# Kernel optimization log

Measured on AMD Instinct MI355X. Metric: run time of the kernel, lower is better.

The kernel has to match this reference:

```python
import jax, jax.numpy as jnp
import numpy as np

B, IMG, TXT, N, FF, HID, C, E = 1024, 512, 300, 14, 2048, 128, 14, 182
D = IMG + TXT  # 812, transformer d_model


def setup_inputs() -> dict:
    key = jax.random.key(0)
    ks = jax.random.split(key, 12)
    r = lambda k, s, sc=0.02: (jax.random.normal(k, s, jnp.float32) * sc)
    return {
        "img_feat": jax.random.normal(ks[0], (B, IMG), jnp.float32),
        "word_embeds": jax.random.normal(ks[1], (N, TXT), jnp.float32),
        "edge_index": jax.random.randint(ks[2], (2, E), 0, N, jnp.int32),
        "in_proj_w": r(ks[3], (3 * D, D)),
        "in_proj_b": jnp.zeros((3 * D,), jnp.float32),
        "out_proj_w": r(ks[4], (D, D)),
        "out_proj_b": jnp.zeros((D,), jnp.float32),
        "ln1_g": jnp.ones((D,), jnp.float32), "ln1_b": jnp.zeros((D,), jnp.float32),
        "ln2_g": jnp.ones((D,), jnp.float32), "ln2_b": jnp.zeros((D,), jnp.float32),
        "ffn_w1": r(ks[5], (D, FF)), "ffn_b1": jnp.zeros((FF,), jnp.float32),
        "ffn_w2": r(ks[6], (FF, D)), "ffn_b2": jnp.zeros((D,), jnp.float32),
        "gcn1_w": r(ks[7], (D, HID)), "gcn1_b": jnp.zeros((HID,), jnp.float32),
        "gcn2_w": r(ks[8], (HID, HID)), "gcn2_b": jnp.zeros((HID,), jnp.float32),
        "lin_w": r(ks[9], (HID, C)), "lin_b": jnp.zeros((C,), jnp.float32),
    }


def layer_norm(x, g, b, eps=1e-5):
    mu = x.mean(-1, keepdims=True)
    var = ((x - mu) ** 2).mean(-1, keepdims=True)
    return (x - mu) * jax.lax.rsqrt(var + eps) * g + b


def gcn_conv(x, edge_index, W, b, n_nodes):
    # PyG GCNConv: add self loops, symmetric normalization, x @ W then scatter-add.
    # x: (B, N, F_in); gather/scatter along node axis (node_dim=-2).
    src, dst = edge_index[0], edge_index[1]
    loop = jnp.arange(n_nodes, dtype=src.dtype)
    src = jnp.concatenate([src, loop])
    dst = jnp.concatenate([dst, loop])
    deg = jnp.zeros((n_nodes,), x.dtype).at[dst].add(1.0)
    dinv = jnp.where(deg > 0, deg ** -0.5, 0.0)
    ew = dinv[src] * dinv[dst]                       # (E+N,)
    h = x @ W                                        # (B, N, F_out)
    msg = h[:, src, :] * ew[None, :, None]           # gather neighbors
    out = jnp.zeros_like(h).at[:, dst, :].add(msg)   # scatter-aggregate
    return out + b


def reference(img_feat, word_embeds, edge_index,
              in_proj_w, in_proj_b, out_proj_w, out_proj_b,
              ln1_g, ln1_b, ln2_g, ln2_b,
              ffn_w1, ffn_b1, ffn_w2, ffn_b2,
              gcn1_w, gcn1_b, gcn2_w, gcn2_b, lin_w, lin_b):
    # Broadcast image feature across the 14 label nodes; concat word embeddings.
    node = jnp.concatenate([
        jnp.broadcast_to(img_feat[:, None, :], (B, N, IMG)),
        jnp.broadcast_to(word_embeds[None, :, :], (B, N, TXT)),
    ], axis=-1)                                      # (B, N, D)

    # torch TransformerEncoderLayer, batch_first=False, nhead=1, post-norm, relu.
    # Input (B, N, D) is interpreted as (seq=B, batch=N, D): attention over dim 0.
    qkv = node @ in_proj_w.T + in_proj_b
    q, k, v = jnp.split(qkv, 3, axis=-1)             # each (B, N, D)
    scale = 1.0 / jnp.sqrt(jnp.asarray(D, node.dtype))
    scores = jnp.einsum('lnd,mnd->nlm', q, k) * scale  # (N, B, B)
    attn = jax.nn.softmax(scores, axis=-1)
    ao = jnp.einsum('nlm,mnd->lnd', attn, v)           # (B, N, D)
    ao = ao @ out_proj_w.T + out_proj_b
    x = layer_norm(node + ao, ln1_g, ln1_b)
    ff = jax.nn.relu(x @ ffn_w1 + ffn_b1) @ ffn_w2 + ffn_b2
    x = layer_norm(x + ff, ln2_g, ln2_b)               # (B, N, D)

    # Two GCNConv layers over the 14-node label graph (batched over B).
    x = jax.nn.relu(gcn_conv(x, edge_index, gcn1_w, gcn1_b, N))
    x = gcn_conv(x, edge_index, gcn2_w, gcn2_b, N)
    x = jax.nn.relu(x.mean(axis=1))                    # mean over nodes -> (B, HID)
    return x @ lin_w + lin_b                           # (B, C)
```

## Files before the change

### kernel.cpp

```cpp
#include <hip/hip_runtime.h>
#include <math.h>

#define B_    1024
#define IMG_  512
#define TXT_  300
#define NN_   14
#define FF_   2048
#define HID_  128
#define CC_   14
#define EE_   182
#define DD_   812
#define D3_   2436
#define BNR_  14336
#define KP_   832
#define TXP_  320
#define AROWS_ 1152

typedef __bf16 bf16x8 __attribute__((ext_vector_type(8)));
typedef float  f32x4  __attribute__((ext_vector_type(4)));
typedef unsigned short u16;

__device__ __forceinline__ u16 f2bf(float f) {
    union { float f; unsigned u; } v; v.f = f;
    unsigned r = v.u + 0x7FFFu + ((v.u >> 16) & 1u);
    return (u16)(r >> 16);
}
__device__ __forceinline__ float bf2f(u16 h) {
    union { unsigned u; float f; } v; v.u = ((unsigned)h) << 16; return v.f;
}

__device__ __forceinline__ void gload_lds16(const u16* g, u16* l) {
    __builtin_amdgcn_global_load_lds(
        (const __attribute__((address_space(1))) void*)g,
        (__attribute__((address_space(3))) void*)l, 16, 0, 0);
}

#define OFF_IMGB  0ULL
#define OFF_WIB   1048576ULL
#define OFF_WORDB 3543040ULL
#define OFF_WITX  3624960ULL
#define OFF_GB    0ULL
#define OFF_EBUF  29360128ULL
#define OFF_AVOT  33611776ULL
#define OFF_WOB   35446784ULL
#define OFF_HB    0ULL
#define OFF_PB    58720256ULL
#define OFF_X1B   82001920ULL
#define OFF_YB    105857024ULL
#define OFF_W1T   129712128ULL
#define OFF_W2T   133120000ULL
#define OFF_AQB   152420352ULL
#define OFF_TVB   158307552ULL
#define OFF_CO    158520544ULL
#define OFF_Z     158566016ULL
#define OFF_ADJ   158623360ULL
#define OFF_WG1T  158624384ULL
#define OFF_WG2T  158837376ULL

__device__ __forceinline__ void gemm_body(
    const u16* __restrict__ A, int lda,
    const u16* __restrict__ Bm, int ldb,
    int M, int N, int K, float scale,
    float* __restrict__ Cf, int ldc,
    u16* __restrict__ Cb, int ldcb,
    const float* __restrict__ bias,
    int nxt, int swiz, int epi, int id)
{
    __shared__ __align__(16) u16 As[2][128 * 32];
    __shared__ __align__(16) u16 Bs[2][128 * 32];
    const int tid = threadIdx.x;
    int bx, by;
    if (swiz) { int r8 = id & 7; int q = id >> 3; bx = q % nxt; by = (q / nxt) * 8 + r8; }
    else      { bx = id % nxt; by = id / nxt; }
    const int row0 = by * 128, col0 = bx * 128;
    const int lane = tid & 63, wv = tid >> 6;
    const int wm = (wv >> 1) * 32, wn = (wv & 1) * 64;
    const int fr = lane & 15, qd = lane >> 4;

    const int s_row = tid >> 2;
    const int s_ko  = (tid & 3) * 8;
    const int s_b0  = wv * 512;
    const u16* Arow = A  + (size_t)(row0 + s_row) * lda + s_ko;
    const u16* Brow = Bm + (size_t)(col0 + s_row) * ldb + s_ko;

    f32x4 acc[2][4] = {};

    const int T = K >> 5;
    gload_lds16(Arow, &As[0][s_b0]);
    gload_lds16(Brow, &Bs[0][s_b0]);

    for (int i = 0; i < T; ++i) {
        __syncthreads();
        const int cur = i & 1;
        if (i + 1 < T) {
            const int ko = (i + 1) << 5;
            gload_lds16(Arow + ko, &As[cur ^ 1][s_b0]);
            gload_lds16(Brow + ko, &Bs[cur ^ 1][s_b0]);
        }
        bf16x8 af[2], bg[4];
        #pragma unroll
        for (int j = 0; j < 2; ++j)
            af[j] = *(const bf16x8*)&As[cur][(wm + j * 16 + fr) * 32 + qd * 8];
        #pragma unroll
        for (int j = 0; j < 4; ++j)
            bg[j] = *(const bf16x8*)&Bs[cur][(wn + j * 16 + fr) * 32 + qd * 8];
        #pragma unroll
        for (int mi = 0; mi < 2; ++mi)
            #pragma unroll
            for (int ni = 0; ni < 4; ++ni)
                acc[mi][ni] = __builtin_amdgcn_mfma_f32_16x16x32_bf16(
                    af[mi], bg[ni], acc[mi][ni], 0, 0, 0);
    }

    #pragma unroll
    for (int mi = 0; mi < 2; ++mi) {
        #pragma unroll
        for (int i = 0; i < 4; ++i) {
            int rm = row0 + wm + mi * 16 + qd * 4 + i;
            if (rm >= M) continue;
            #pragma unroll
            for (int ni = 0; ni < 4; ++ni) {
                int cn = col0 + wn + ni * 16 + fr;
                if (cn >= N) continue;
                float v = acc[mi][ni][i] * scale;
                if (epi == 0) Cf[(size_t)rm * ldc + cn] = v;
                else if (epi == 1) { v += bias[cn]; v = v > 0.f ? v : 0.f;
                                Cb[(size_t)rm * ldcb + cn] = f2bf(v); }
                else if (epi == 2) Cf[(size_t)rm * ldc + cn] =
                                v + bias[cn] + bf2f(Cb[(size_t)rm * ldcb + cn]);
                else if (epi == 3) Cb[(size_t)rm * ldcb + cn] = f2bf(v);
                else if (epi == 4) { int bs = cn / DD_, cc = cn - bs * DD_;
                                Cb[(size_t)bs * (AROWS_ * KP_) + (size_t)rm * KP_ + cc] = f2bf(v); }
                else if (epi == 5) { float invz = 1.0f / bias[rm];
                                Cb[(size_t)rm * ldcb + cn] = f2bf(v * invz); }
                else if (epi == 6) Cf[(size_t)rm * ldc + cn] = v + bias[cn];
                else if (epi == 7) { const u16* rx = (const u16*)Cf;
                                Cb[(size_t)rm * ldcb + cn] =
                                    f2bf(v + bias[cn] + bf2f(rx[(size_t)rm * ldc + cn])); }
                else if (epi == 8) {
                    float t = v + bias[cn];
                    if (cn < DD_) Cb[(size_t)(1024 + rm) * KP_ + cn] = f2bf(t);
                    else if (cn >= 2 * DD_)
                        ((u16*)Cf)[(size_t)rm * KP_ + (cn - 2 * DD_)] = f2bf(t);
                }
            }
        }
    }
}

template<int EPI>
__global__ __launch_bounds__(512, 6)
void bgemm(const u16* __restrict__ A, int lda,
           const u16* __restrict__ Bm, int ldb,
           int M, int N, int K, float scale,
           float* __restrict__ Cf, int ldc,
           u16* __restrict__ Cb, int ldcb,
           const float* __restrict__ bias,
           int nxt, int swiz)
{
    gemm_body(A, lda, Bm, ldb, M, N, K, scale, Cf, ldc, Cb, ldcb, bias,
              nxt, swiz, EPI, blockIdx.x);
}

struct GDesc {
    const u16* A; const u16* B; float* Cf; u16* Cb; const float* bias;
    int lda, ldb, ldc, ldcb, M, N, K, epi, nxt, swiz, blk0;
    float scale;
};
struct TDesc { const float* src; u16* dst; int srs, drs, rows, cols, padrows, rt, nblk; };
struct MPack { GDesc g[3]; TDesc t[2]; const int* ei; float* Adj; int ng, gtot, nt; };

__device__ __forceinline__ void castT_body(TDesc T, int id)
{
    __shared__ float t[32][33];
    const int bx = id % T.rt, by = id / T.rt;
    const int r0 = bx * 32, c0 = by * 32;
    const int tx = threadIdx.x & 31, ty = threadIdx.x >> 5;
    #pragma unroll
    for (int k = 0; k < 2; ++k) {
        int r = r0 + ty + k * 16, c = c0 + tx;
        t[ty + k * 16][tx] = (r < T.rows && c < T.cols) ? T.src[(size_t)r * T.srs + c] : 0.f;
    }
    __syncthreads();
    #pragma unroll
    for (int k = 0; k < 2; ++k) {
        int c = c0 + ty + k * 16, r = r0 + tx;
        if (c < T.cols && r < T.padrows)
            T.dst[(size_t)c * T.drs + r] = f2bf(t[tx][ty + k * 16]);
    }
}

__device__ __forceinline__ void adj_body(const int* __restrict__ ei, float* __restrict__ Adj)
{
    if (threadIdx.x != 0) return;
    float deg[NN_];
    for (int i = 0; i < NN_; ++i) deg[i] = 1.f;
    for (int e = 0; e < EE_; ++e) deg[ei[EE_ + e]] += 1.f;
    float dinv[NN_];
    for (int i = 0; i < NN_; ++i) dinv[i] = rsqrtf(deg[i]);
    float adj[NN_ * NN_];
    for (int t = 0; t < NN_ * NN_; ++t) adj[t] = 0.f;
    for (int e = 0; e < EE_; ++e) {
        int s = ei[e], d = ei[EE_ + e];
        adj[d * NN_ + s] += dinv[s] * dinv[d];
    }
    for (int i = 0; i < NN_; ++i) adj[i * NN_ + i] += dinv[i] * dinv[i];
    for (int t = 0; t < NN_ * NN_; ++t) Adj[t] = adj[t];
    for (int i = 0; i < 16; ++i) {
        float s = 0.f;
        if (i < NN_) for (int j = 0; j < NN_; ++j) s += adj[j * NN_ + i];
        Adj[NN_ * NN_ + i] = s / (float)NN_;
    }
}

__global__ __launch_bounds__(512, 6)
void kern_mix(MPack p)
{
    int id = blockIdx.x;
    if (id < p.gtot) {
        int si = 0;
        for (int s = 1; s < p.ng; ++s) if (id >= p.g[s].blk0) si = s;
        GDesc D = p.g[si];
        gemm_body(D.A, D.lda, D.B, D.ldb, D.M, D.N, D.K, D.scale,
                  D.Cf, D.ldc, D.Cb, D.ldcb, D.bias, D.nxt, D.swiz, D.epi,
                  id - D.blk0);
        return;
    }
    id -= p.gtot;
    for (int s = 0; s < p.nt; ++s) {
        if (id < p.t[s].nblk) { castT_body(p.t[s], id); return; }
        id -= p.t[s].nblk;
    }
    if (id == 0 && p.ei) adj_body(p.ei, p.Adj);
}

struct CDesc { const float* src; u16* dst; int srs, drs, dcols, scols; };
struct CPack { CDesc d[9]; unsigned cum[10]; int n; };

__global__ void kern_mcast(CPack p)
{
    unsigned idx = blockIdx.x * 256 + threadIdx.x;
    int si = -1;
    for (int s = 0; s < p.n; ++s)
        if (idx >= p.cum[s] && idx < p.cum[s + 1]) { si = s; break; }
    if (si < 0) return;
    CDesc D = p.d[si];
    unsigned k = idx - p.cum[si];
    int r = k / D.dcols, c = k - r * D.dcols;
    D.dst[(size_t)r * D.drs + c] =
        (c < D.scols) ? f2bf(D.src[(size_t)r * D.srs + c]) : (u16)0;
}

__global__ __launch_bounds__(256) void kern_eG(const float* __restrict__ S,
    u16* __restrict__ Gb, float* __restrict__ Z)
{
    __shared__ float red[256];
    __shared__ u16 ews[NN_ * 1024];
    const int l = blockIdx.x, tid = threadIdx.x;
    const int lane = tid & 63, wv = tid >> 6;

    const float* wraw = S + 1024 * 1024;
    for (int z = wv; z < NN_; z += 4) {
        const float* r = wraw + z * 1024;
        float vv[16], mx = -1e30f;
        #pragma unroll
        for (int j = 0; j < 16; ++j) { vv[j] = r[lane + 64 * j]; mx = fmaxf(mx, vv[j]); }
        #pragma unroll
        for (int off = 32; off > 0; off >>= 1) mx = fmaxf(mx, __shfl_down(mx, off));
        mx = __shfl(mx, 0);
        #pragma unroll
        for (int j = 0; j < 16; ++j)
            ews[z * 1024 + lane + 64 * j] = f2bf(expf(vv[j] - mx));
    }
    const float* row = S + (size_t)l * 1024;
    float m = -1e30f;
    #pragma unroll
    for (int k = 0; k < 4; ++k) m = fmaxf(m, row[tid + 256 * k]);
    red[tid] = m; __syncthreads();
    for (int s = 128; s > 0; s >>= 1) {
        if (tid < s) red[tid] = fmaxf(red[tid], red[tid + s]);
        __syncthreads();
    }
    m = red[0];
    float ev[16];
    #pragma unroll
    for (int j = 0; j < 16; ++j) ev[j] = expf(row[lane + 64 * j] - m);
    u16* gr = Gb + (size_t)l * NN_ * 1024;
    for (int z = wv; z < NN_; z += 4) {
        const u16* er = &ews[z * 1024];
        float s = 0.f;
        #pragma unroll
        for (int j = 0; j < 16; ++j) {
            float pv = ev[j] * bf2f(er[lane + 64 * j]);
            gr[(size_t)z * 1024 + lane + 64 * j] = f2bf(pv);
            s += pv;
        }
        #pragma unroll
        for (int off = 32; off > 0; off >>= 1) s += __shfl_down(s, off);
        if (lane == 0) Z[l * NN_ + z] = s;
    }
}

__global__ __launch_bounds__(256) void kern_ln1(
    const float* __restrict__ img, const float* __restrict__ word,
    const u16* __restrict__ Pb,
    const float* __restrict__ co, const float* __restrict__ g,
    const float* __restrict__ bta, u16* __restrict__ Xb)
{
    __shared__ float buf[DD_];
    __shared__ float red[256];
    __shared__ float stats[2];
    int row = blockIdx.x;
    int b = row / NN_, n = row - b * NN_;
    const u16* pr = Pb + (size_t)row * DD_;
    const float* cr = co + n * DD_;
    float s = 0.f;
    for (int d = threadIdx.x; d < DD_; d += 256) {
        float v = (d < IMG_) ? img[(size_t)b * IMG_ + d] : word[n * TXT_ + d - IMG_];
        v += bf2f(pr[d]) + cr[d];
        buf[d] = v; s += v;
    }
    red[threadIdx.x] = s; __syncthreads();
    for (int t = 128; t > 0; t >>= 1) {
        if (threadIdx.x < t) red[threadIdx.x] += red[threadIdx.x + t];
        __syncthreads();
    }
    if (threadIdx.x == 0) stats[0] = red[0] / DD_;
    __syncthreads();
    float mu = stats[0], s2 = 0.f;
    for (int d = threadIdx.x; d < DD_; d += 256) { float t = buf[d] - mu; s2 += t * t; }
    red[threadIdx.x] = s2; __syncthreads();
    for (int t = 128; t > 0; t >>= 1) {
        if (threadIdx.x < t) red[threadIdx.x] += red[threadIdx.x + t];
        __syncthreads();
    }
    if (threadIdx.x == 0) stats[1] = rsqrtf(red[0] / DD_ + 1e-5f);
    __syncthreads();
    float rstd = stats[1];
    u16* xb = Xb + (size_t)row * KP_;
    for (int d = threadIdx.x; d < DD_; d += 256)
        xb[d] = f2bf((buf[d] - mu) * rstd * g[d] + bta[d]);
    for (int d = DD_ + threadIdx.x; d < KP_; d += 256) xb[d] = 0;
}

#define X2S_ 840
#define G1S_ 136
__global__ __launch_bounds__(256, 4)
void kern_gcn(const u16* __restrict__ Yb,
              const float* __restrict__ g2v, const float* __restrict__ bt2,
              const u16* __restrict__ Wg1T, const float* __restrict__ bg1,
              const u16* __restrict__ Wg2T, const float* __restrict__ bg2,
              const float* __restrict__ Wl,  const float* __restrict__ bl,
              const float* __restrict__ AdjW, float* __restrict__ out)
{
    __shared__ __align__(16) u16 x2s[16 * X2S_];
    __shared__ __align__(16) float h1s[16 * 132];
    __shared__ float adj_s[NN_ * NN_];
    __shared__ float colw_s[16];
    __shared__ float pool_s[HID_];
    u16* g1s = x2s;
    const int b = blockIdx.x, tid = threadIdx.x;
    const int lane = tid & 63, wv = tid >> 6;
    const int fr = lane & 15, qd = lane >> 4;

    if (tid < NN_ * NN_) adj_s[tid] = AdjW[tid];
    if (tid >= NN_ * NN_ && tid < NN_ * NN_ + 16) colw_s[tid - NN_ * NN_] = AdjW[tid];
    for (int k = tid; k < 2 * X2S_; k += 256) x2s[14 * X2S_ + k] = 0;
    for (int k = tid; k < 14 * (X2S_ - DD_); k += 256) {
        int j = k / (X2S_ - DD_), c = k - j * (X2S_ - DD_);
        x2s[j * X2S_ + DD_ + c] = 0;
    }

    for (int j = wv; j < NN_; j += 4) {
        const u16* yr = Yb + (size_t)(b * NN_ + j) * KP_;
        float vv[13], s = 0.f;
        #pragma unroll
        for (int k = 0; k < 13; ++k) {
            int d = lane + 64 * k;
            float v = (d < DD_) ? bf2f(yr[d]) : 0.f;
            vv[k] = v; s += v;
        }
        #pragma unroll
        for (int off = 32; off > 0; off >>= 1) s += __shfl_down(s, off);
        s = __shfl(s, 0);
        float mu = s / (float)DD_, s2 = 0.f;
        #pragma unroll
        for (int k = 0; k < 13; ++k) {
            int d = lane + 64 * k;
            float t = (d < DD_) ? vv[k] - mu : 0.f;
            s2 += t * t;
        }
        #pragma unroll
        for (int off = 32; off > 0; off >>= 1) s2 += __shfl_down(s2, off);
        s2 = __shfl(s2, 0);
        float rstd = rsqrtf(s2 / (float)DD_ + 1e-5f);
        #pragma unroll
        for (int k = 0; k < 13; ++k) {
            int d = lane + 64 * k;
            if (d < DD_)
                x2s[j * X2S_ + d] = f2bf((vv[k] - mu) * rstd * g2v[d] + bt2[d]);
        }
    }
    __syncthreads();

    {
        f32x4 acc[2] = {{}, {}};
        const u16* wp0 = Wg1T + (size_t)(wv * 32 + fr) * KP_ + qd * 8;
        const u16* wp1 = wp0 + (size_t)16 * KP_;
        bf16x8 bc0 = *(const bf16x8*)wp0;
        bf16x8 bc1 = *(const bf16x8*)wp1;
        for (int k0 = 0; k0 < KP_; k0 += 32) {
            bf16x8 bn0 = bc0, bn1 = bc1;
            if (k0 + 32 < KP_) {
                bn0 = *(const bf16x8*)(wp0 + k0 + 32);
                bn1 = *(const bf16x8*)(wp1 + k0 + 32);
            }
            bf16x8 af = *(const bf16x8*)&x2s[fr * X2S_ + k0 + qd * 8];
            acc[0] = __builtin_amdgcn_mfma_f32_16x16x32_bf16(af, bc0, acc[0], 0, 0, 0);
            acc[1] = __builtin_amdgcn_mfma_f32_16x16x32_bf16(af, bc1, acc[1], 0, 0, 0);
            bc0 = bn0; bc1 = bn1;
        }
        #pragma unroll
        for (int t = 0; t < 2; ++t)
            #pragma unroll
            for (int i = 0; i < 4; ++i)
                h1s[(qd * 4 + i) * 132 + wv * 32 + t * 16 + fr] = acc[t][i];
    }
    __syncthreads();

    {
        const int f = tid & 127, jj = (tid >> 7) * 7;
        #pragma unroll
        for (int j = 0; j < 7; ++j) {
            float s = bg1[f];
            #pragma unroll
            for (int i = 0; i < NN_; ++i)
                s = fmaf(adj_s[(jj + j) * NN_ + i], h1s[i * 132 + f], s);
            g1s[(jj + j) * G1S_ + f] = f2bf(s > 0.f ? s : 0.f);
        }
        for (int k = tid; k < 2 * G1S_; k += 256) g1s[14 * G1S_ + k] = 0;
    }
    __syncthreads();

    {
        f32x4 acc[2] = {{}, {}};
        const u16* wp0 = Wg2T + (size_t)(wv * 32 + fr) * HID_ + qd * 8;
        const u16* wp1 = wp0 + (size_t)16 * HID_;
        bf16x8 bc0 = *(const bf16x8*)wp0;
        bf16x8 bc1 = *(const bf16x8*)wp1;
        for (int k0 = 0; k0 < HID_; k0 += 32) {
            bf16x8 bn0 = bc0, bn1 = bc1;
            if (k0 + 32 < HID_) {
                bn0 = *(const bf16x8*)(wp0 + k0 + 32);
                bn1 = *(const bf16x8*)(wp1 + k0 + 32);
            }
            bf16x8 af = *(const bf16x8*)&g1s[fr * G1S_ + k0 + qd * 8];
            acc[0] = __builtin_amdgcn_mfma_f32_16x16x32_bf16(af, bc0, acc[0], 0, 0, 0);
            acc[1] = __builtin_amdgcn_mfma_f32_16x16x32_bf16(af, bc1, acc[1], 0, 0, 0);
            bc0 = bn0; bc1 = bn1;
        }
        #pragma unroll
        for (int t = 0; t < 2; ++t) {
            float s = 0.f;
            #pragma unroll
            for (int i = 0; i < 4; ++i) s += colw_s[qd * 4 + i] * acc[t][i];
            s += __shfl_xor(s, 16);
            s += __shfl_xor(s, 32);
            if (qd == 0) {
                int f = wv * 32 + t * 16 + fr;
                float p = s + bg2[f];
                pool_s[f] = p > 0.f ? p : 0.f;
            }
        }
    }
    __syncthreads();

    if (tid < CC_) {
        float s = bl[tid];
        #pragma unroll 8
        for (int f = 0; f < HID_; ++f)
            s = fmaf(pool_s[f], Wl[(size_t)f * CC_ + tid], s);
        out[(size_t)b * CC_ + tid] = s;
    }
}

extern "C" void kernel_launch(void* const* d_in, const int* in_sizes, int n_in,
                              void* d_out, int out_size, void* d_ws, size_t ws_size,
                              hipStream_t stream)
{
    const float* img  = (const float*)d_in[0];
    const float* word = (const float*)d_in[1];
    const int*   ei   = (const int*)d_in[2];
    const float* Wi   = (const float*)d_in[3];
    const float* bi   = (const float*)d_in[4];
    const float* Wo   = (const float*)d_in[5];
    const float* bo   = (const float*)d_in[6];
    const float* g1   = (const float*)d_in[7];
    const float* bt1  = (const float*)d_in[8];
    const float* g2   = (const float*)d_in[9];
    const float* bt2  = (const float*)d_in[10];
    const float* W1   = (const float*)d_in[11];
    const float* bf1  = (const float*)d_in[12];
    const float* W2   = (const float*)d_in[13];
    const float* bf2  = (const float*)d_in[14];
    const float* Wg1  = (const float*)d_in[15];
    const float* bg1  = (const float*)d_in[16];
    const float* Wg2  = (const float*)d_in[17];
    const float* bg2  = (const float*)d_in[18];
    const float* Wl   = (const float*)d_in[19];
    const float* bl   = (const float*)d_in[20];
    float* out = (float*)d_out;

    char* ws = (char*)d_ws;
    u16*   imgb = (u16*)  (ws + OFF_IMGB);
    u16*   Wib  = (u16*)  (ws + OFF_WIB);
    u16*   wordb= (u16*)  (ws + OFF_WORDB);
    u16*   WiTX = (u16*)  (ws + OFF_WITX);
    u16*   Gb   = (u16*)  (ws + OFF_GB);
    float* Ebuf = (float*)(ws + OFF_EBUF);
    u16*   AvoT = (u16*)  (ws + OFF_AVOT);
    u16*   Wob  = (u16*)  (ws + OFF_WOB);
    u16*   Hb   = (u16*)  (ws + OFF_HB);
    u16*   Pb   = (u16*)  (ws + OFF_PB);
    u16*   X1b  = (u16*)  (ws + OFF_X1B);
    u16*   Yb   = (u16*)  (ws + OFF_YB);
    u16*   W1T  = (u16*)  (ws + OFF_W1T);
    u16*   W2T  = (u16*)  (ws + OFF_W2T);
    u16*   Aqb  = (u16*)  (ws + OFF_AQB);
    u16*   Akb  = Aqb + AROWS_ * KP_;
    u16*   Avb  = Aqb + 2 * AROWS_ * KP_;
    u16*   Tvb  = (u16*)  (ws + OFF_TVB);
    float* co   = (float*)(ws + OFF_CO);
    float* Zb   = (float*)(ws + OFF_Z);
    float* Adj  = (float*)(ws + OFF_ADJ);
    u16*   Wg1T = (u16*)  (ws + OFF_WG1T);
    u16*   Wg2T = (u16*)  (ws + OFF_WG2T);

    const float scl = 1.0f / sqrtf((float)DD_);

    {
        CPack p; p.n = 9;
        unsigned c = 0;
        auto seg = [&](int i, const float* s, int srs, u16* d, int drs,
                       int rows, int dcols, int scols) {
            p.d[i] = { s, d, srs, drs, dcols, scols };
            p.cum[i] = c; c += (unsigned)rows * dcols;
        };
        seg(0, img,        IMG_, imgb,  IMG_, B_,   IMG_, IMG_);
        seg(1, Wi,         DD_,  Wib,   IMG_, D3_,  IMG_, IMG_);
        seg(2, word,       TXT_, wordb, TXP_, NN_,  TXP_, TXT_);
        seg(3, Wi + IMG_,  DD_,  WiTX,  TXP_, D3_,  TXP_, TXT_);
        seg(4, Wo,         DD_,  Wob,   KP_,  DD_,  KP_,  DD_);
        seg(5, nullptr, 0, Aqb + DD_,                    KP_, 1038, 20, 0);
        seg(6, nullptr, 0, Aqb + AROWS_ * KP_ + DD_,     KP_, 1024, 20, 0);
        seg(7, nullptr, 0, Aqb + 2 * AROWS_ * KP_ + DD_, KP_, 1024, 20, 0);
        seg(8, nullptr, 0, Tvb + DD_,                    KP_, NN_,  20, 0);
        p.cum[9] = c;
        kern_mcast<<<(c + 255) / 256, 256, 0, stream>>>(p);
    }

    {
        MPack p{};
        p.ng = 2; p.gtot = 180;
        p.g[0] = { wordb, WiTX, (float*)Tvb, Aqb, bi,
                   TXP_, TXP_, 0, 0, NN_, D3_, TXP_, 8, 20, 0, 0, 1.f };
        p.g[1] = { imgb, Wib, nullptr, Aqb, nullptr,
                   IMG_, IMG_, 0, 0, B_, D3_, IMG_, 4, 20, 1, 20, 1.f };
        p.nt = 2;
        p.t[0] = { Wg1, Wg1T, HID_, KP_,  DD_,  HID_, KP_,  26, 26 * 4 };
        p.t[1] = { Wg2, Wg2T, HID_, HID_, HID_, HID_, HID_, 4,  4 * 4 };
        p.ei = ei; p.Adj = Adj;
        kern_mix<<<180 + 104 + 16 + 1, 512, 0, stream>>>(p);
    }

    {
        MPack p{};
        p.ng = 3; p.gtot = 135;
        p.g[0] = { Aqb, Akb, Ebuf, nullptr, nullptr,
                   KP_, KP_, 1024, 0, 1024 + NN_, 1024, KP_, 0, 8, 0, 0, scl };
        p.g[1] = { Wob, Avb, nullptr, AvoT, nullptr,
                   KP_, KP_, 0, 1024, DD_, B_, KP_, 3, 8, 0, 72, 1.f };
        p.g[2] = { Tvb, Wob, co, nullptr, bo,
                   KP_, KP_, DD_, 0, NN_, DD_, KP_, 6, 7, 0, 128, 1.f };
        p.nt = 2;
        p.t[0] = { W1, W1T, FF_, KP_, DD_, FF_, KP_, 26, 26 * 64 };
        p.t[1] = { W2, W2T, DD_, FF_, FF_, DD_, FF_, 64, 64 * 26 };
        p.ei = nullptr; p.Adj = nullptr;
        kern_mix<<<135 + 1664 + 1664, 512, 0, stream>>>(p);
    }

    kern_eG<<<1024, 256, 0, stream>>>(Ebuf, Gb, Zb);

    bgemm<5><<<7 * 112, 512, 0, stream>>>(Gb, 1024, AvoT, 1024,
        BNR_, DD_, 1024, 1.f, nullptr, 0, Pb, DD_, Zb, 7, 1);

    kern_ln1<<<BNR_, 256, 0, stream>>>(img, word, Pb, co, g1, bt1, X1b);

    bgemm<1><<<16 * 112, 512, 0, stream>>>(X1b, KP_, W1T, KP_,
        BNR_, FF_, KP_, 1.f, nullptr, 0, Hb, FF_, bf1, 16, 1);
    bgemm<7><<<7 * 112, 512, 0, stream>>>(Hb, FF_, W2T, FF_,
        BNR_, DD_, FF_, 1.f, (float*)X1b, KP_, Yb, KP_, bf2, 7, 1);

    kern_gcn<<<B_, 256, 0, stream>>>(Yb, g2, bt2, Wg1T, bg1, Wg2T, bg2,
                                     Wl, bl, Adj, out);
}
```

Measured before the change: 532.4 us.

## Use 4-wave 128x128 GEMM tiles with 64x64 per-wave subtiles for big GEMMs

Result: faster. 456.7 us (-14.2%).

```diff
diff --git a/kernel.cpp b/kernel.cpp
--- a/kernel.cpp
+++ b/kernel.cpp
@@ -57,7 +57,111 @@
 #define OFF_WG1T  158624384ULL
 #define OFF_WG2T  158837376ULL
 
-__device__ __forceinline__ void gemm_body(
+__device__ __forceinline__ void gemm_epi(
+    float v, int rm, int cn, int epi,
+    float* __restrict__ Cf, int ldc, u16* __restrict__ Cb, int ldcb,
+    const float* __restrict__ bias)
+{
+    if (epi == 0) Cf[(size_t)rm * ldc + cn] = v;
+    else if (epi == 1) { v += bias[cn]; v = v > 0.f ? v : 0.f;
+                    Cb[(size_t)rm * ldcb + cn] = f2bf(v); }
+    else if (epi == 2) Cf[(size_t)rm * ldc + cn] =
+                    v + bias[cn] + bf2f(Cb[(size_t)rm * ldcb + cn]);
+    else if (epi == 3) Cb[(size_t)rm * ldcb + cn] = f2bf(v);
+    else if (epi == 4) { int bs = cn / DD_, cc = cn - bs * DD_;
+                    Cb[(size_t)bs * (AROWS_ * KP_) + (size_t)rm * KP_ + cc] = f2bf(v); }
+    else if (epi == 5) { float invz = 1.0f / bias[rm];
+                    Cb[(size_t)rm * ldcb + cn] = f2bf(v * invz); }
+    else if (epi == 6) Cf[(size_t)rm * ldc + cn] = v + bias[cn];
+    else if (epi == 7) { const u16* rx = (const u16*)Cf;
+                    Cb[(size_t)rm * ldcb + cn] =
+                        f2bf(v + bias[cn] + bf2f(rx[(size_t)rm * ldc + cn])); }
+    else if (epi == 8) {
+        float t = v + bias[cn];
+        if (cn < DD_) Cb[(size_t)(1024 + rm) * KP_ + cn] = f2bf(t);
+        else if (cn >= 2 * DD_)
+            ((u16*)Cf)[(size_t)rm * KP_ + (cn - 2 * DD_)] = f2bf(t);
+    }
+}
+
+__device__ __forceinline__ void gemm_body4(
+    const u16* __restrict__ A, int lda,
+    const u16* __restrict__ Bm, int ldb,
+    int M, int N, int K, float scale,
+    float* __restrict__ Cf, int ldc,
+    u16* __restrict__ Cb, int ldcb,
+    const float* __restrict__ bias,
+    int nxt, int swiz, int epi, int id)
+{
+    __shared__ __align__(16) u16 As[2][128 * 32];
+    __shared__ __align__(16) u16 Bs[2][128 * 32];
+    const int tid = threadIdx.x;
+    int bx, by;
+    if (swiz) { int r8 = id & 7; int q = id >> 3; bx = q % nxt; by = (q / nxt) * 8 + r8; }
+    else      { bx = id % nxt; by = id / nxt; }
+    const int row0 = by * 128, col0 = bx * 128;
+    const int lane = tid & 63, wv = tid >> 6;
+    const int wm = (wv >> 1) * 64, wn = (wv & 1) * 64;
+    const int fr = lane & 15, qd = lane >> 4;
+
+    const int s_r0  = (wv * 64 + lane) >> 2;
+    const int s_ko  = (lane & 3) * 8;
+    const int s_b0  = (wv * 64) * 8;
+    const u16* Arow0 = A  + (size_t)(row0 + s_r0) * lda + s_ko;
+    const u16* Arow1 = A  + (size_t)(row0 + s_r0 + 64) * lda + s_ko;
+    const u16* Brow0 = Bm + (size_t)(col0 + s_r0) * ldb + s_ko;
+    const u16* Brow1 = Bm + (size_t)(col0 + s_r0 + 64) * ldb + s_ko;
+
+    f32x4 acc[4][4] = {};
+
+    const int T = K >> 5;
+    gload_lds16(Arow0, &As[0][s_b0]);
+    gload_lds16(Arow1, &As[0][s_b0 + 2048]);
+    gload_lds16(Brow0, &Bs[0][s_b0]);
+    gload_lds16(Brow1, &Bs[0][s_b0 + 2048]);
+
+    for (int i = 0; i < T; ++i) {
+        __syncthreads();
+        const int cur = i & 1;
+        if (i + 1 < T) {
+            const int nb = cur ^ 1;
+            const int ko = (i + 1) << 5;
+            gload_lds16(Arow0 + ko, &As[nb][s_b0]);
+            gload_lds16(Arow1 + ko, &As[nb][s_b0 + 2048]);
+            gload_lds16(Brow0 + ko, &Bs[nb][s_b0]);
+            gload_lds16(Brow1 + ko, &Bs[nb][s_b0 + 2048]);
+        }
+        bf16x8 af[4], bg[4];
+        #pragma unroll
+        for (int j = 0; j < 4; ++j) {
+            af[j] = *(const bf16x8*)&As[cur][(wm + j * 16 + fr) * 32 + qd * 8];
+            bg[j] = *(const bf16x8*)&Bs[cur][(wn + j * 16 + fr) * 32 + qd * 8];
+        }
+        #pragma unroll
+        for (int mi = 0; mi < 4; ++mi)
+            #pragma unroll
+            for (int ni = 0; ni < 4; ++ni)
+                acc[mi][ni] = __builtin_amdgcn_mfma_f32_16x16x32_bf16(
+                    af[mi], bg[ni], acc[mi][ni], 0, 0, 0);
+    }
+
+    #pragma unroll
+    for (int mi = 0; mi < 4; ++mi) {
+        #pragma unroll
+        for (int i = 0; i < 4; ++i) {
+            int rm = row0 + wm + mi * 16 + qd * 4 + i;
+            if (rm >= M) continue;
+            #pragma unroll
+            for (int ni = 0; ni < 4; ++ni) {
+                int cn = col0 + wn + ni * 16 + fr;
+                if (cn >= N) continue;
+                gemm_epi(acc[mi][ni][i] * scale, rm, cn, epi, Cf, ldc, Cb, ldcb, bias);
+            }
+        }
+    }
+}
+
+__device__ __forceinline__ void gemm_body8(
     const u16* __restrict__ A, int lda,
     const u16* __restrict__ Bm, int ldb,
     int M, int N, int K, float scale,
@@ -77,9 +181,9 @@
     const int wm = (wv >> 1) * 32, wn = (wv & 1) * 64;
     const int fr = lane & 15, qd = lane >> 4;
 
+    const int s_b0  = wv * 512;
     const int s_row = tid >> 2;
     const int s_ko  = (tid & 3) * 8;
-    const int s_b0  = wv * 512;
     const u16* Arow = A  + (size_t)(row0 + s_row) * lda + s_ko;
     const u16* Brow = Bm + (size_t)(col0 + s_row) * ldb + s_ko;
 
@@ -122,34 +226,14 @@
             for (int ni = 0; ni < 4; ++ni) {
                 int cn = col0 + wn + ni * 16 + fr;
                 if (cn >= N) continue;
-                float v = acc[mi][ni][i] * scale;
-                if (epi == 0) Cf[(size_t)rm * ldc + cn] = v;
-                else if (epi == 1) { v += bias[cn]; v = v > 0.f ? v : 0.f;
-                                Cb[(size_t)rm * ldcb + cn] = f2bf(v); }
-                else if (epi == 2) Cf[(size_t)rm * ldc + cn] =
-                                v + bias[cn] + bf2f(Cb[(size_t)rm * ldcb + cn]);
-                else if (epi == 3) Cb[(size_t)rm * ldcb + cn] = f2bf(v);
-                else if (epi == 4) { int bs = cn / DD_, cc = cn - bs * DD_;
-                                Cb[(size_t)bs * (AROWS_ * KP_) + (size_t)rm * KP_ + cc] = f2bf(v); }
-                else if (epi == 5) { float invz = 1.0f / bias[rm];
-                                Cb[(size_t)rm * ldcb + cn] = f2bf(v * invz); }
-                else if (epi == 6) Cf[(size_t)rm * ldc + cn] = v + bias[cn];
-                else if (epi == 7) { const u16* rx = (const u16*)Cf;
-                                Cb[(size_t)rm * ldcb + cn] =
-                                    f2bf(v + bias[cn] + bf2f(rx[(size_t)rm * ldc + cn])); }
-                else if (epi == 8) {
-                    float t = v + bias[cn];
-                    if (cn < DD_) Cb[(size_t)(1024 + rm) * KP_ + cn] = f2bf(t);
-                    else if (cn >= 2 * DD_)
-                        ((u16*)Cf)[(size_t)rm * KP_ + (cn - 2 * DD_)] = f2bf(t);
-                }
+                gemm_epi(acc[mi][ni][i] * scale, rm, cn, epi, Cf, ldc, Cb, ldcb, bias);
             }
         }
     }
 }
 
 template<int EPI>
-__global__ __launch_bounds__(512, 6)
+__global__ __launch_bounds__(256, 4)
 void bgemm(const u16* __restrict__ A, int lda,
            const u16* __restrict__ Bm, int ldb,
            int M, int N, int K, float scale,
@@ -158,8 +242,8 @@
            const float* __restrict__ bias,
            int nxt, int swiz)
 {
-    gemm_body(A, lda, Bm, ldb, M, N, K, scale, Cf, ldc, Cb, ldcb, bias,
-              nxt, swiz, EPI, blockIdx.x);
+    gemm_body4(A, lda, Bm, ldb, M, N, K, scale, Cf, ldc, Cb, ldcb, bias,
+               nxt, swiz, EPI, blockIdx.x);
 }
 
 struct GDesc {
@@ -192,24 +276,25 @@
 
 __device__ __forceinline__ void adj_body(const int* __restrict__ ei, float* __restrict__ Adj)
 {
-    if (threadIdx.x != 0) return;
-    float deg[NN_];
-    for (int i = 0; i < NN_; ++i) deg[i] = 1.f;
-    for (int e = 0; e < EE_; ++e) deg[ei[EE_ + e]] += 1.f;
-    float dinv[NN_];
-    for (int i = 0; i < NN_; ++i) dinv[i] = rsqrtf(deg[i]);
-    float adj[NN_ * NN_];
-    for (int t = 0; t < NN_ * NN_; ++t) adj[t] = 0.f;
-    for (int e = 0; e < EE_; ++e) {
-        int s = ei[e], d = ei[EE_ + e];
-        adj[d * NN_ + s] += dinv[s] * dinv[d];
-    }
-    for (int i = 0; i < NN_; ++i) adj[i * NN_ + i] += dinv[i] * dinv[i];
-    for (int t = 0; t < NN_ * NN_; ++t) Adj[t] = adj[t];
-    for (int i = 0; i < 16; ++i) {
-        float s = 0.f;
-        if (i < NN_) for (int j = 0; j < NN_; ++j) s += adj[j * NN_ + i];
-        Adj[NN_ * NN_ + i] = s / (float)NN_;
+    __shared__ float degS[NN_], dinvS[NN_], adjS[NN_ * NN_];
+    const int tid = threadIdx.x;
+    if (tid < NN_) degS[tid] = 1.f;
+    if (tid < NN_ * NN_) adjS[tid] = 0.f;
+    __syncthreads();
+    int s = 0, d = 0;
+    if (tid < EE_) { s = ei[tid]; d = ei[EE_ + tid]; atomicAdd(&degS[d], 1.f); }
+    __syncthreads();
+    if (tid < NN_) dinvS[tid] = rsqrtf(degS[tid]);
+    __syncthreads();
+    if (tid < EE_) atomicAdd(&adjS[d * NN_ + s], dinvS[s] * dinvS[d]);
+    if (tid < NN_) atomicAdd(&adjS[tid * NN_ + tid], dinvS[tid] * dinvS[tid]);
+    __syncthreads();
+    if (tid < NN_ * NN_) Adj[tid] = adjS[tid];
+    if (tid < 16) {
+        float sum = 0.f;
+        if (tid < NN_)
+            for (int j = 0; j < NN_; ++j) sum += adjS[j * NN_ + tid];
+        Adj[NN_ * NN_ + tid] = sum / (float)NN_;
     }
 }
 
@@ -221,9 +306,9 @@
         int si = 0;
         for (int s = 1; s < p.ng; ++s) if (id >= p.g[s].blk0) si = s;
         GDesc D = p.g[si];
-        gemm_body(D.A, D.lda, D.B, D.ldb, D.M, D.N, D.K, D.scale,
-                  D.Cf, D.ldc, D.Cb, D.ldcb, D.bias, D.nxt, D.swiz, D.epi,
-                  id - D.blk0);
+        gemm_body8(D.A, D.lda, D.B, D.ldb, D.M, D.N, D.K, D.scale,
+                   D.Cf, D.ldc, D.Cb, D.ldcb, D.bias, D.nxt, D.swiz, D.epi,
+                   id - D.blk0);
         return;
     }
     id -= p.gtot;
@@ -591,14 +676,14 @@
 
     kern_eG<<<1024, 256, 0, stream>>>(Ebuf, Gb, Zb);
 
-    bgemm<5><<<7 * 112, 512, 0, stream>>>(Gb, 1024, AvoT, 1024,
+    bgemm<5><<<7 * 112, 256, 0, stream>>>(Gb, 1024, AvoT, 1024,
         BNR_, DD_, 1024, 1.f, nullptr, 0, Pb, DD_, Zb, 7, 1);
 
     kern_ln1<<<BNR_, 256, 0, stream>>>(img, word, Pb, co, g1, bt1, X1b);
 
-    bgemm<1><<<16 * 112, 512, 0, stream>>>(X1b, KP_, W1T, KP_,
+    bgemm<1><<<16 * 112, 256, 0, stream>>>(X1b, KP_, W1T, KP_,
         BNR_, FF_, KP_, 1.f, nullptr, 0, Hb, FF_, bf1, 16, 1);
-    bgemm<7><<<7 * 112, 512, 0, stream>>>(Hb, FF_, W2T, FF_,
+    bgemm<7><<<7 * 112, 256, 0, stream>>>(Hb, FF_, W2T, FF_,
         BNR_, DD_, FF_, 1.f, (float*)X1b, KP_, Yb, KP_, bf2, 7, 1);
 
     kern_gcn<<<B_, 256, 0, stream>>>(Yb, g2, bt2, Wg1T, bg1, Wg2T, bg2,
```
